# Performance work log

Hardware: AMD Instinct MI355X
Metric: run time of the kernel (lower is better)

Reference implementation:

```python
import jax, jax.numpy as jnp
import numpy as np

D = 512          # input_dim == hidden size of MinLSTM layers
OUT = 1          # output_dim of fc_out
B, T = 8, 4096
LN_EPS = 1e-5


def _linear_params(key, d_in, d_out):
    kw, kb = jax.random.split(key)
    lim = 1.0 / np.sqrt(d_in)
    W = jax.random.uniform(kw, (d_out, d_in), minval=-lim, maxval=lim, dtype=jnp.float32)
    b = jax.random.uniform(kb, (d_out,), minval=-lim, maxval=lim, dtype=jnp.float32)
    return W, b


def setup_inputs() -> dict:
    key = jax.random.key(0)
    ks = jax.random.split(key, 8)
    x = jax.random.normal(ks[0], (B, T, D), dtype=jnp.float32)
    Wf0, bf0 = _linear_params(ks[1], D, D)
    Wi0, bi0 = _linear_params(ks[2], D, D)
    Wh0, bh0 = _linear_params(ks[3], D, D)
    Wf1, bf1 = _linear_params(ks[4], D, D)
    Wi1, bi1 = _linear_params(ks[5], D, D)
    Wh1, bh1 = _linear_params(ks[6], D, D)
    W_out, b_out = _linear_params(ks[7], D, OUT)
    ln_g = jnp.ones((D,), dtype=jnp.float32)
    ln_b = jnp.zeros((D,), dtype=jnp.float32)
    return {
        'x': x,
        'Wf0': Wf0, 'bf0': bf0, 'Wi0': Wi0, 'bi0': bi0, 'Wh0': Wh0, 'bh0': bh0,
        'Wf1': Wf1, 'bf1': bf1, 'Wi1': Wi1, 'bi1': bi1, 'Wh1': Wh1, 'bh1': bh1,
        'ln_g': ln_g, 'ln_b': ln_b, 'W_out': W_out, 'b_out': b_out,
    }


def _minlstm(x, Wf, bf, Wi, bi, Wh, bh):
    # minLSTM (parallel form, h0 = 0):
    #   f = sigma(W_f x), i = sigma(W_i x), h~ = W_h x
    #   f' = f/(f+i), i' = i/(f+i)
    #   h_t = f'_t * h_{t-1} + i'_t * h~_t   (linear recurrence -> associative scan)
    f = jax.nn.sigmoid(jnp.einsum('btd,ed->bte', x, Wf) + bf)
    i = jax.nn.sigmoid(jnp.einsum('btd,ed->bte', x, Wi) + bi)
    h_tilde = jnp.einsum('btd,ed->bte', x, Wh) + bh
    denom = f + i
    a = f / denom                      # decay coefficient f'
    u = (i / denom) * h_tilde          # input contribution i' * h~

    def combine(c1, c2):
        a1, u1 = c1
        a2, u2 = c2
        return a1 * a2, a2 * u1 + u2

    _, h = jax.lax.associative_scan(combine, (a, u), axis=1)
    return h  # [B, T, D]


def reference(x, Wf0, bf0, Wi0, bi0, Wh0, bh0,
              Wf1, bf1, Wi1, bi1, Wh1, bh1,
              ln_g, ln_b, W_out, b_out):
    h = _minlstm(x, Wf0, bf0, Wi0, bi0, Wh0, bh0)
    h = _minlstm(h, Wf1, bf1, Wi1, bi1, Wh1, bh1)
    h = jnp.where(jnp.isnan(h), x, h)      # NaN fallback to input
    h = x + h                               # residual
    # LayerNorm over last dim
    mu = jnp.mean(h, axis=-1, keepdims=True)
    var = jnp.mean(jnp.square(h - mu), axis=-1, keepdims=True)
    hn = (h - mu) * jax.lax.rsqrt(var + LN_EPS) * ln_g + ln_b
    # output projection [B, T, OUT]
    return jnp.einsum('btd,od->bto', hn, W_out) + b_out
```

## Files before the change

### kernel.cpp

```cpp
#include <hip/hip_runtime.h>
#include <hip/hip_bf16.h>
#include <stdint.h>


#define MROWS 32768
#define DDIM  512
#define TLEN  4096
#define BSZ   8
#define NCHUNK 64
#define CLEN   64

typedef __attribute__((ext_vector_type(8))) __bf16 bf16x8;
typedef __attribute__((ext_vector_type(4))) float f32x4;
typedef __attribute__((ext_vector_type(4))) unsigned short ushort4_t;

static __device__ __forceinline__ unsigned short f2bf(float f) {
    unsigned int u = __float_as_uint(f);
    u = (u + 0x7FFFu + ((u >> 16) & 1u)) >> 16;
    return (unsigned short)u;
}
static __device__ __forceinline__ float bf2f(unsigned short s) {
    return __uint_as_float(((unsigned int)s) << 16);
}
static __device__ __forceinline__ void gload_lds16(const void* gptr, void* ldsp) {
    __builtin_amdgcn_global_load_lds(
        (const __attribute__((address_space(1))) uint32_t*)gptr,
        (__attribute__((address_space(3))) uint32_t*)ldsp,
        16, 0, 0);
}

#define WAITV(n) asm volatile("s_waitcnt vmcnt(" #n ")" ::: "memory")

__global__ __launch_bounds__(256) void cast_all(
    const float4* __restrict__ x,
    const float4* __restrict__ w0, const float4* __restrict__ w1,
    const float4* __restrict__ w2, const float4* __restrict__ w3,
    const float4* __restrict__ w4, const float4* __restrict__ w5,
    ushort4_t* __restrict__ xb, ushort4_t* __restrict__ wb)
{
    int i = blockIdx.x * 256 + threadIdx.x;
    float4 v;
    ushort4_t* dst;
    if (i < 4194304) {
        v = x[i];
        dst = xb + i;
    } else {
        int j = i - 4194304;
        int wsel = j >> 16;
        int rem = j & 65535;
        const float4* src = (wsel == 0) ? w0 : (wsel == 1) ? w1 : (wsel == 2) ? w2
                          : (wsel == 3) ? w3 : (wsel == 4) ? w4 : w5;
        v = src[rem];
        dst = wb + j;
    }
    ushort4_t o;
    o.x = f2bf(v.x); o.y = f2bf(v.y); o.z = f2bf(v.z); o.w = f2bf(v.w);
    *dst = o;
}

__global__ __launch_bounds__(512, 4) void gates_gemm(
    const unsigned short* __restrict__ X,
    const unsigned short* __restrict__ Wf,
    const unsigned short* __restrict__ Wi,
    const unsigned short* __restrict__ Wh,
    const float* __restrict__ bf_, const float* __restrict__ bi_,
    const float* __restrict__ bh_,
    unsigned int* __restrict__ au_out,
    float* __restrict__ Asum, float* __restrict__ Usum)
{
    __shared__ __align__(16) unsigned short lds[2 * 10240];

    const int tid  = threadIdx.x;
    const int lane = tid & 63;
    const int wave = tid >> 6;
    const int wm = wave >> 1;
    const int wn = wave & 1;
    const int lr  = lane & 15;
    const int kgl = lane >> 4;

    const int w = blockIdx.x;
    const int xcd = w & 7;
    const int s = w >> 3;
    const int by = xcd * 32 + (s >> 3);
    const int bx = s & 7;
    const int mblk = by * 128;
    const int nblk = bx * 64;

    const int r4 = lane >> 2;
    const int c4 = lane & 3;
    const unsigned short *g0, *g1, *g2;
    int o0, o1, o2;
    {
        const int sb = (wave < 4) ? wave * 3 : 12 + (wave - 4) * 2;
        const int sl2 = (wave < 4) ? sb + 2 : sb + 1;
        const int sls[3] = {sb, sb + 1, sl2};
        const unsigned short* gp[3];
        int of[3];
#pragma unroll
        for (int i = 0; i < 3; ++i) {
            int sl = sls[i];
            const unsigned short* src;
            int lrow, grow;
            if (sl < 8)       { src = X;  lrow = sl * 16 + r4;        grow = mblk + lrow; }
            else if (sl < 12) { src = Wf; lrow = (sl - 8) * 16 + r4;  grow = nblk + lrow; }
            else if (sl < 16) { src = Wi; lrow = (sl - 12) * 16 + r4; grow = nblk + lrow; }
            else              { src = Wh; lrow = (sl - 16) * 16 + r4; grow = nblk + lrow; }
            int cg = ((c4 ^ (lrow >> 1)) & 3) << 3;
            gp[i] = src + (size_t)grow * 512 + cg;
            of[i] = sl * 512 + r4 * 32 + c4 * 8;
        }
        g0 = gp[0]; g1 = gp[1]; g2 = gp[2];
        o0 = of[0]; o1 = of[1]; o2 = of[2];
    }

    int aoff[2], boff[2];
#pragma unroll
    for (int mi = 0; mi < 2; ++mi) {
        int row = wm * 32 + mi * 16 + lr;
        aoff[mi] = row * 32 + (((kgl ^ (row >> 1)) & 3) << 3);
    }
#pragma unroll
    for (int ni = 0; ni < 2; ++ni) {
        int row = wn * 32 + ni * 16 + lr;
        boff[ni] = 4096 + row * 32 + (((kgl ^ (row >> 1)) & 3) << 3);
    }

    f32x4 accF[2][2], accI[2][2], accH[2][2];
    const f32x4 zero = {0.f, 0.f, 0.f, 0.f};
#pragma unroll
    for (int mi = 0; mi < 2; ++mi)
#pragma unroll
        for (int ni = 0; ni < 2; ++ni) {
            accF[mi][ni] = zero; accI[mi][ni] = zero; accH[mi][ni] = zero;
        }

#define STAGE(bb) do { \
    gload_lds16(g0, lds + (bb) + o0); \
    gload_lds16(g1, lds + (bb) + o1); \
    if (wave < 4) gload_lds16(g2, lds + (bb) + o2); \
    g0 += 32; g1 += 32; g2 += 32; } while (0)

    STAGE(0);

#pragma unroll
    for (int t = 0; t < 16; ++t) {
        if (t < 15) {
            STAGE(((t + 1) & 1) * 10240);
            if (wave < 4) { WAITV(3); } else { WAITV(2); }
        } else {
            WAITV(0);
        }
        __builtin_amdgcn_s_barrier();
        __builtin_amdgcn_sched_barrier(0);

        const unsigned short* cb = lds + (t & 1) * 10240;
        bf16x8 af[2];
#pragma unroll
        for (int mi = 0; mi < 2; ++mi)
            af[mi] = *reinterpret_cast<const bf16x8*>(cb + aoff[mi]);
        bf16x8 bF[2], bI[2], bH[2];
#pragma unroll
        for (int ni = 0; ni < 2; ++ni) {
            bF[ni] = *reinterpret_cast<const bf16x8*>(cb + boff[ni]);
            bI[ni] = *reinterpret_cast<const bf16x8*>(cb + 2048 + boff[ni]);
            bH[ni] = *reinterpret_cast<const bf16x8*>(cb + 4096 + boff[ni]);
        }
        __builtin_amdgcn_s_setprio(1);
#pragma unroll
        for (int mi = 0; mi < 2; ++mi)
#pragma unroll
            for (int ni = 0; ni < 2; ++ni) {
                accF[mi][ni] = __builtin_amdgcn_mfma_f32_16x16x32_bf16(af[mi], bF[ni], accF[mi][ni], 0, 0, 0);
                accI[mi][ni] = __builtin_amdgcn_mfma_f32_16x16x32_bf16(af[mi], bI[ni], accI[mi][ni], 0, 0, 0);
                accH[mi][ni] = __builtin_amdgcn_mfma_f32_16x16x32_bf16(af[mi], bH[ni], accH[mi][ni], 0, 0, 0);
            }
        __builtin_amdgcn_s_setprio(0);
        __builtin_amdgcn_sched_barrier(0);
        __builtin_amdgcn_s_barrier();
        __builtin_amdgcn_sched_barrier(0);
    }
#undef STAGE

    float pa[2], pu[2];
#pragma unroll
    for (int ni = 0; ni < 2; ++ni) {
        const int n = nblk + wn * 32 + ni * 16 + lr;
        const float bfv = bf_[n], biv = bi_[n], bhv = bh_[n];
        float ca = 1.f, cu = 0.f;
#pragma unroll
        for (int mi = 0; mi < 2; ++mi) {
            float sa = 1.f, su = 0.f;
#pragma unroll
            for (int r = 0; r < 4; ++r) {
                const int m = mblk + wm * 32 + mi * 16 + kgl * 4 + r;
                float zf = accF[mi][ni][r] + bfv;
                float zi = accI[mi][ni][r] + biv;
                float zh = accH[mi][ni][r] + bhv;
                float ef = __expf(-zf);
                float ei = __expf(-zi);
                float inv = __frcp_rn(2.0f + ef + ei);
                float av = (1.0f + ei) * inv;
                float uv = (1.0f + ef) * inv * zh;
                au_out[(size_t)m * 512 + n] =
                    ((unsigned int)f2bf(uv) << 16) | (unsigned int)f2bf(av);
                sa *= av; su = av * su + uv;
            }
            float oa = __shfl_xor(sa, 16), ou = __shfl_xor(su, 16);
            bool up = (lane & 16) != 0;
            float ta = sa * oa;
            float tu = up ? (sa * ou + su) : (oa * su + ou);
            sa = ta; su = tu;
            oa = __shfl_xor(sa, 32); ou = __shfl_xor(su, 32);
            up = (lane & 32) != 0;
            ta = sa * oa;
            tu = up ? (sa * ou + su) : (oa * su + ou);
            sa = ta; su = tu;
            cu = sa * cu + su; ca = ca * sa;
        }
        pa[ni] = ca; pu[ni] = cu;
    }
    float* sm = (float*)lds;
    if (kgl == 0) {
#pragma unroll
        for (int ni = 0; ni < 2; ++ni) {
            int nl = wn * 32 + ni * 16 + lr;
            sm[wm * 64 + nl] = pa[ni];
            sm[256 + wm * 64 + nl] = pu[ni];
        }
    }
    __syncthreads();
    if (tid < 128) {
        int cl = tid >> 6, nl = tid & 63;
        float a1 = sm[(2 * cl) * 64 + nl],     u1 = sm[256 + (2 * cl) * 64 + nl];
        float a2 = sm[(2 * cl + 1) * 64 + nl], u2 = sm[256 + (2 * cl + 1) * 64 + nl];
        size_t ci = (size_t)(by * 2 + cl) * 512 + nblk + nl;
        Asum[ci] = a1 * a2;
        Usum[ci] = a2 * u1 + u2;
    }
}

__global__ void scan_pass2(const float4* __restrict__ Asum, const float4* __restrict__ Usum,
                           float4* __restrict__ Hinit) {
    int t = blockIdx.x * 256 + threadIdx.x;
    int d4 = t & 127;
    int b = t >> 7;
    float4 h = {0.f, 0.f, 0.f, 0.f};
    for (int c = 0; c < NCHUNK; ++c) {
        size_t idx = (size_t)(b * NCHUNK + c) * 128 + d4;
        Hinit[idx] = h;
        float4 A = Asum[idx]; float4 U = Usum[idx];
        h.x = A.x * h.x + U.x; h.y = A.y * h.y + U.y;
        h.z = A.z * h.z + U.z; h.w = A.w * h.w + U.w;
    }
}

__global__ void scan_pass3(const uint4* __restrict__ au,
                           const float4* __restrict__ Hinit,
                           ushort4_t* __restrict__ hout) {
    int gid = blockIdx.x * 256 + threadIdx.x;
    int d4 = gid & 127;
    int c  = (gid >> 7) & 63;
    int b  = gid >> 13;
    size_t base = (size_t)(b * TLEN + c * CLEN) * 128 + d4;
    size_t s4 = (size_t)(b * NCHUNK + c) * 128 + d4;
    float4 h0 = Hinit[s4];
    float h[4] = {h0.x, h0.y, h0.z, h0.w};
#pragma unroll 4
    for (int l = 0; l < CLEN; ++l) {
        size_t idx = base + (size_t)l * 128;
        uint4 v = au[idx];
        unsigned int vv[4] = {v.x, v.y, v.z, v.w};
        ushort4_t o;
#pragma unroll
        for (int j = 0; j < 4; ++j) {
            float av = __uint_as_float(vv[j] << 16);
            float uv = __uint_as_float(vv[j] & 0xFFFF0000u);
            h[j] = av * h[j] + uv;
            o[j] = f2bf(h[j]);
        }
        hout[idx] = o;
    }
}

__global__ __launch_bounds__(128) void scan3_final(
    const uint4* __restrict__ au, const float4* __restrict__ Hinit,
    const float4* __restrict__ x4,
    const float* __restrict__ g, const float* __restrict__ bvec,
    const float* __restrict__ Wout, const float* __restrict__ bout,
    float* __restrict__ out)
{
    const int blk = blockIdx.x;
    const int b = blk >> 6, c = blk & 63;
    const int d4 = threadIdx.x;
    const int lane = threadIdx.x & 63;
    const int wv = threadIdx.x >> 6;

    float4 h0 = Hinit[(size_t)blk * 128 + d4];
    float h[4] = {h0.x, h0.y, h0.z, h0.w};
    float4 g4 = reinterpret_cast<const float4*>(g)[d4];
    float4 b4 = reinterpret_cast<const float4*>(bvec)[d4];
    float4 w4 = reinterpret_cast<const float4*>(Wout)[d4];
    const float ga[4] = {g4.x, g4.y, g4.z, g4.w};
    const float ba[4] = {b4.x, b4.y, b4.z, b4.w};
    const float wa[4] = {w4.x, w4.y, w4.z, w4.w};
    const float bo = bout[0];

    __shared__ float redS[2], redQ[2], redP[2];
    size_t base = ((size_t)b * TLEN + c * CLEN) * 128 + d4;

    for (int l = 0; l < CLEN; ++l) {
        size_t idx = base + (size_t)l * 128;
        uint4 v = au[idx];
        float4 xr = x4[idx];
        const unsigned int vv[4] = {v.x, v.y, v.z, v.w};
        const float xa[4] = {xr.x, xr.y, xr.z, xr.w};
        float r[4];
        float sfl = 0.f, q = 0.f;
#pragma unroll
        for (int j = 0; j < 4; ++j) {
            float av = __uint_as_float(vv[j] << 16);
            float uv = __uint_as_float(vv[j] & 0xFFFF0000u);
            h[j] = av * h[j] + uv;
            float hv = h[j];
            if (hv != hv) hv = xa[j];
            float rr = xa[j] + hv;
            r[j] = rr;
            sfl += rr; q += rr * rr;
        }
#pragma unroll
        for (int m = 32; m >= 1; m >>= 1) {
            sfl += __shfl_xor(sfl, m);
            q += __shfl_xor(q, m);
        }
        if (lane == 0) { redS[wv] = sfl; redQ[wv] = q; }
        __syncthreads();
        float st = redS[0] + redS[1];
        float qt = redQ[0] + redQ[1];
        float mu = st * (1.0f / 512.0f);
        float var = qt * (1.0f / 512.0f) - mu * mu;
        float rstd = rsqrtf(var + 1e-5f);
        float p = 0.f;
#pragma unroll
        for (int j = 0; j < 4; ++j)
            p += ((r[j] - mu) * rstd * ga[j] + ba[j]) * wa[j];
#pragma unroll
        for (int m = 32; m >= 1; m >>= 1) p += __shfl_xor(p, m);
        if (lane == 0) redP[wv] = p;
        __syncthreads();
        if (threadIdx.x == 0)
            out[(size_t)b * TLEN + c * CLEN + l] = redP[0] + redP[1] + bo;
    }
}

extern "C" void kernel_launch(void* const* d_in, const int* in_sizes, int n_in,
                              void* d_out, int out_size, void* d_ws, size_t ws_size,
                              hipStream_t stream) {
    const float* x    = (const float*)d_in[0];
    const float* Wf0  = (const float*)d_in[1];  const float* bf0 = (const float*)d_in[2];
    const float* Wi0  = (const float*)d_in[3];  const float* bi0 = (const float*)d_in[4];
    const float* Wh0  = (const float*)d_in[5];  const float* bh0 = (const float*)d_in[6];
    const float* Wf1  = (const float*)d_in[7];  const float* bf1 = (const float*)d_in[8];
    const float* Wi1  = (const float*)d_in[9];  const float* bi1 = (const float*)d_in[10];
    const float* Wh1  = (const float*)d_in[11]; const float* bh1 = (const float*)d_in[12];
    const float* ln_g = (const float*)d_in[13]; const float* ln_b = (const float*)d_in[14];
    const float* W_out = (const float*)d_in[15]; const float* b_out = (const float*)d_in[16];

    char* ws = (char*)d_ws;
    unsigned short* Xb = (unsigned short*)ws;  ws += (size_t)MROWS * DDIM * 2;
    unsigned short* Wball = (unsigned short*)ws;
    unsigned short* Wb[6];
    for (int i = 0; i < 6; ++i) { Wb[i] = (unsigned short*)ws; ws += (size_t)DDIM * DDIM * 2; }
    unsigned int* aubuf = (unsigned int*)ws; ws += (size_t)MROWS * DDIM * 4;
    float* Asum = (float*)ws;  ws += (size_t)BSZ * NCHUNK * DDIM * 4;
    float* Usum = (float*)ws;  ws += (size_t)BSZ * NCHUNK * DDIM * 4;
    float* Hinit = (float*)ws; ws += (size_t)BSZ * NCHUNK * DDIM * 4;
    unsigned short* h0b = (unsigned short*)ws; ws += (size_t)MROWS * DDIM * 2;

    cast_all<<<17920, 256, 0, stream>>>(
        (const float4*)x, (const float4*)Wf0, (const float4*)Wi0, (const float4*)Wh0,
        (const float4*)Wf1, (const float4*)Wi1, (const float4*)Wh1,
        (ushort4_t*)Xb, (ushort4_t*)Wball);

    gates_gemm<<<2048, 512, 0, stream>>>(Xb, Wb[0], Wb[1], Wb[2], bf0, bi0, bh0,
                                         aubuf, Asum, Usum);
    scan_pass2<<<4, 256, 0, stream>>>((const float4*)Asum, (const float4*)Usum, (float4*)Hinit);
    scan_pass3<<<256, 256, 0, stream>>>((const uint4*)aubuf, (const float4*)Hinit, (ushort4_t*)h0b);

    gates_gemm<<<2048, 512, 0, stream>>>(h0b, Wb[3], Wb[4], Wb[5], bf1, bi1, bh1,
                                         aubuf, Asum, Usum);
    scan_pass2<<<4, 256, 0, stream>>>((const float4*)Asum, (const float4*)Usum, (float4*)Hinit);
    scan3_final<<<512, 128, 0, stream>>>((const uint4*)aubuf, (const float4*)Hinit,
                                         (const float4*)x, ln_g, ln_b, W_out, b_out,
                                         (float*)d_out);
}
```

Baseline: 246.5 us.

## Switch gates GEMM to 32x32x16 MFMA with 4 waves per block

Rewrites the gates GEMM to use 256-thread blocks (4 waves), with each wave computing a 64x32 tile via 32x32x16 bf16 MFMA instead of 16x16x32, and restructures LDS staging so each thread issues five uniform 16-byte loads. Each wave now owns a full 64-row chunk, so the chunk scan summary is written straight from registers without the shared-memory combine and extra block barrier. The aim is fewer LDS fragment reads per FLOP and less epilogue sync. The cost is more accumulator registers per wave and fewer waves per block for latency hiding.

```diff
diff --git a/kernel.cpp b/kernel.cpp
--- a/kernel.cpp
+++ b/kernel.cpp
@@ -11,7 +11,7 @@
 #define CLEN   64
 
 typedef __attribute__((ext_vector_type(8))) __bf16 bf16x8;
-typedef __attribute__((ext_vector_type(4))) float f32x4;
+typedef __attribute__((ext_vector_type(16))) float f32x16;
 typedef __attribute__((ext_vector_type(4))) unsigned short ushort4_t;
 
 static __device__ __forceinline__ unsigned short f2bf(float f) {
@@ -58,7 +58,7 @@
     *dst = o;
 }
 
-__global__ __launch_bounds__(512, 4) void gates_gemm(
+__global__ __launch_bounds__(256, 3) void gates_gemm(
     const unsigned short* __restrict__ X,
     const unsigned short* __restrict__ Wf,
     const unsigned short* __restrict__ Wi,
@@ -75,8 +75,8 @@
     const int wave = tid >> 6;
     const int wm = wave >> 1;
     const int wn = wave & 1;
-    const int lr  = lane & 15;
-    const int kgl = lane >> 4;
+    const int ln31 = lane & 31;
+    const int kh = lane >> 5;
 
     const int w = blockIdx.x;
     const int xcd = w & 7;
@@ -86,59 +86,45 @@
     const int mblk = by * 128;
     const int nblk = bx * 64;
 
-    const int r4 = lane >> 2;
-    const int c4 = lane & 3;
-    const unsigned short *g0, *g1, *g2;
-    int o0, o1, o2;
+    const int srow = tid >> 2;
+    const int c4   = tid & 3;
+    const int cg   = ((c4 ^ ((srow >> 1) & 3)) << 3);
+    const int tid8 = tid * 8;
+    const unsigned short* g0 = X  + (size_t)(mblk + srow) * 512 + cg;
+    const unsigned short* g1 = X  + (size_t)(mblk + 64 + srow) * 512 + cg;
+    const unsigned short* g2 = Wf + (size_t)(nblk + srow) * 512 + cg;
+    const unsigned short* g3 = Wi + (size_t)(nblk + srow) * 512 + cg;
+    const unsigned short* g4 = Wh + (size_t)(nblk + srow) * 512 + cg;
+
+    int aoff[2][2], boff[2];
+#pragma unroll
+    for (int mi = 0; mi < 2; ++mi) {
+        int row = wm * 64 + mi * 32 + ln31;
+#pragma unroll
+        for (int ks = 0; ks < 2; ++ks)
+            aoff[mi][ks] = row * 32 + (((2 * ks + kh) ^ ((row >> 1) & 3)) << 3);
+    }
     {
-        const int sb = (wave < 4) ? wave * 3 : 12 + (wave - 4) * 2;
-        const int sl2 = (wave < 4) ? sb + 2 : sb + 1;
-        const int sls[3] = {sb, sb + 1, sl2};
-        const unsigned short* gp[3];
-        int of[3];
-#pragma unroll
-        for (int i = 0; i < 3; ++i) {
-            int sl = sls[i];
-            const unsigned short* src;
-            int lrow, grow;
-            if (sl < 8)       { src = X;  lrow = sl * 16 + r4;        grow = mblk + lrow; }
-            else if (sl < 12) { src = Wf; lrow = (sl - 8) * 16 + r4;  grow = nblk + lrow; }
-            else if (sl < 16) { src = Wi; lrow = (sl - 12) * 16 + r4; grow = nblk + lrow; }
-            else              { src = Wh; lrow = (sl - 16) * 16 + r4; grow = nblk + lrow; }
-            int cg = ((c4 ^ (lrow >> 1)) & 3) << 3;
-            gp[i] = src + (size_t)grow * 512 + cg;
-            of[i] = sl * 512 + r4 * 32 + c4 * 8;
-        }
-        g0 = gp[0]; g1 = gp[1]; g2 = gp[2];
-        o0 = of[0]; o1 = of[1]; o2 = of[2];
-    }
-
-    int aoff[2], boff[2];
+        int brow = wn * 32 + ln31;
+#pragma unroll
+        for (int ks = 0; ks < 2; ++ks)
+            boff[ks] = brow * 32 + (((2 * ks + kh) ^ ((brow >> 1) & 3)) << 3);
+    }
+
+    f32x16 accF[2], accI[2], accH[2];
 #pragma unroll
     for (int mi = 0; mi < 2; ++mi) {
-        int row = wm * 32 + mi * 16 + lr;
-        aoff[mi] = row * 32 + (((kgl ^ (row >> 1)) & 3) << 3);
-    }
-#pragma unroll
-    for (int ni = 0; ni < 2; ++ni) {
-        int row = wn * 32 + ni * 16 + lr;
-        boff[ni] = 4096 + row * 32 + (((kgl ^ (row >> 1)) & 3) << 3);
-    }
-
-    f32x4 accF[2][2], accI[2][2], accH[2][2];
-    const f32x4 zero = {0.f, 0.f, 0.f, 0.f};
-#pragma unroll
-    for (int mi = 0; mi < 2; ++mi)
-#pragma unroll
-        for (int ni = 0; ni < 2; ++ni) {
-            accF[mi][ni] = zero; accI[mi][ni] = zero; accH[mi][ni] = zero;
-        }
+#pragma unroll
+        for (int e = 0; e < 16; ++e) { accF[mi][e] = 0.f; accI[mi][e] = 0.f; accH[mi][e] = 0.f; }
+    }
 
 #define STAGE(bb) do { \
-    gload_lds16(g0, lds + (bb) + o0); \
-    gload_lds16(g1, lds + (bb) + o1); \
-    if (wave < 4) gload_lds16(g2, lds + (bb) + o2); \
-    g0 += 32; g1 += 32; g2 += 32; } while (0)
+    gload_lds16(g0, lds + (bb) + tid8);            \
+    gload_lds16(g1, lds + (bb) + 2048 + tid8);     \
+    gload_lds16(g2, lds + (bb) + 4096 + tid8);     \
+    gload_lds16(g3, lds + (bb) + 6144 + tid8);     \
+    gload_lds16(g4, lds + (bb) + 8192 + tid8);     \
+    g0 += 32; g1 += 32; g2 += 32; g3 += 32; g4 += 32; } while (0)
 
     STAGE(0);
 
@@ -146,7 +132,7 @@
     for (int t = 0; t < 16; ++t) {
         if (t < 15) {
             STAGE(((t + 1) & 1) * 10240);
-            if (wave < 4) { WAITV(3); } else { WAITV(2); }
+            WAITV(5);
         } else {
             WAITV(0);
         }
@@ -154,48 +140,45 @@
         __builtin_amdgcn_sched_barrier(0);
 
         const unsigned short* cb = lds + (t & 1) * 10240;
-        bf16x8 af[2];
-#pragma unroll
-        for (int mi = 0; mi < 2; ++mi)
-            af[mi] = *reinterpret_cast<const bf16x8*>(cb + aoff[mi]);
-        bf16x8 bF[2], bI[2], bH[2];
-#pragma unroll
-        for (int ni = 0; ni < 2; ++ni) {
-            bF[ni] = *reinterpret_cast<const bf16x8*>(cb + boff[ni]);
-            bI[ni] = *reinterpret_cast<const bf16x8*>(cb + 2048 + boff[ni]);
-            bH[ni] = *reinterpret_cast<const bf16x8*>(cb + 4096 + boff[ni]);
-        }
-        __builtin_amdgcn_s_setprio(1);
-#pragma unroll
-        for (int mi = 0; mi < 2; ++mi)
-#pragma unroll
-            for (int ni = 0; ni < 2; ++ni) {
-                accF[mi][ni] = __builtin_amdgcn_mfma_f32_16x16x32_bf16(af[mi], bF[ni], accF[mi][ni], 0, 0, 0);
-                accI[mi][ni] = __builtin_amdgcn_mfma_f32_16x16x32_bf16(af[mi], bI[ni], accI[mi][ni], 0, 0, 0);
-                accH[mi][ni] = __builtin_amdgcn_mfma_f32_16x16x32_bf16(af[mi], bH[ni], accH[mi][ni], 0, 0, 0);
+#pragma unroll
+        for (int ks = 0; ks < 2; ++ks) {
+            bf16x8 af[2];
+            af[0] = *reinterpret_cast<const bf16x8*>(cb + aoff[0][ks]);
+            af[1] = *reinterpret_cast<const bf16x8*>(cb + aoff[1][ks]);
+            bf16x8 bF = *reinterpret_cast<const bf16x8*>(cb + 4096 + boff[ks]);
+            bf16x8 bI = *reinterpret_cast<const bf16x8*>(cb + 6144 + boff[ks]);
+            bf16x8 bH = *reinterpret_cast<const bf16x8*>(cb + 8192 + boff[ks]);
+            __builtin_amdgcn_s_setprio(1);
+#pragma unroll
+            for (int mi = 0; mi < 2; ++mi) {
+                accF[mi] = __builtin_amdgcn_mfma_f32_32x32x16_bf16(af[mi], bF, accF[mi], 0, 0, 0);
+                accI[mi] = __builtin_amdgcn_mfma_f32_32x32x16_bf16(af[mi], bI, accI[mi], 0, 0, 0);
+                accH[mi] = __builtin_amdgcn_mfma_f32_32x32x16_bf16(af[mi], bH, accH[mi], 0, 0, 0);
             }
-        __builtin_amdgcn_s_setprio(0);
+            __builtin_amdgcn_s_setprio(0);
+        }
         __builtin_amdgcn_sched_barrier(0);
         __builtin_amdgcn_s_barrier();
         __builtin_amdgcn_sched_barrier(0);
     }
 #undef STAGE
 
-    float pa[2], pu[2];
-#pragma unroll
-    for (int ni = 0; ni < 2; ++ni) {
-        const int n = nblk + wn * 32 + ni * 16 + lr;
-        const float bfv = bf_[n], biv = bi_[n], bhv = bh_[n];
-        float ca = 1.f, cu = 0.f;
-#pragma unroll
-        for (int mi = 0; mi < 2; ++mi) {
+    const int n = nblk + wn * 32 + ln31;
+    const float bfv = bf_[n], biv = bi_[n], bhv = bh_[n];
+    const bool up = (lane & 32) != 0;
+    float ca = 1.f, cu = 0.f;
+#pragma unroll
+    for (int mi = 0; mi < 2; ++mi) {
+#pragma unroll
+        for (int j = 0; j < 4; ++j) {
             float sa = 1.f, su = 0.f;
 #pragma unroll
             for (int r = 0; r < 4; ++r) {
-                const int m = mblk + wm * 32 + mi * 16 + kgl * 4 + r;
-                float zf = accF[mi][ni][r] + bfv;
-                float zi = accI[mi][ni][r] + biv;
-                float zh = accH[mi][ni][r] + bhv;
+                const int reg = 4 * j + r;
+                const int m = mblk + wm * 64 + mi * 32 + 8 * j + 4 * kh + r;
+                float zf = accF[mi][reg] + bfv;
+                float zi = accI[mi][reg] + biv;
+                float zh = accH[mi][reg] + bhv;
                 float ef = __expf(-zf);
                 float ei = __expf(-zi);
                 float inv = __frcp_rn(2.0f + ef + ei);
@@ -203,39 +186,18 @@
                 float uv = (1.0f + ef) * inv * zh;
                 au_out[(size_t)m * 512 + n] =
                     ((unsigned int)f2bf(uv) << 16) | (unsigned int)f2bf(av);
-                sa *= av; su = av * su + uv;
+                su = av * su + uv; sa *= av;
             }
-            float oa = __shfl_xor(sa, 16), ou = __shfl_xor(su, 16);
-            bool up = (lane & 16) != 0;
+            float oa = __shfl_xor(sa, 32), ou = __shfl_xor(su, 32);
             float ta = sa * oa;
             float tu = up ? (sa * ou + su) : (oa * su + ou);
-            sa = ta; su = tu;
-            oa = __shfl_xor(sa, 32); ou = __shfl_xor(su, 32);
-            up = (lane & 32) != 0;
-            ta = sa * oa;
-            tu = up ? (sa * ou + su) : (oa * su + ou);
-            sa = ta; su = tu;
-            cu = sa * cu + su; ca = ca * sa;
-        }
-        pa[ni] = ca; pu[ni] = cu;
-    }
-    float* sm = (float*)lds;
-    if (kgl == 0) {
-#pragma unroll
-        for (int ni = 0; ni < 2; ++ni) {
-            int nl = wn * 32 + ni * 16 + lr;
-            sm[wm * 64 + nl] = pa[ni];
-            sm[256 + wm * 64 + nl] = pu[ni];
-        }
-    }
-    __syncthreads();
-    if (tid < 128) {
-        int cl = tid >> 6, nl = tid & 63;
-        float a1 = sm[(2 * cl) * 64 + nl],     u1 = sm[256 + (2 * cl) * 64 + nl];
-        float a2 = sm[(2 * cl + 1) * 64 + nl], u2 = sm[256 + (2 * cl + 1) * 64 + nl];
-        size_t ci = (size_t)(by * 2 + cl) * 512 + nblk + nl;
-        Asum[ci] = a1 * a2;
-        Usum[ci] = a2 * u1 + u2;
+            cu = ta * cu + tu; ca = ca * ta;
+        }
+    }
+    if (lane < 32) {
+        size_t ci = (size_t)(by * 2 + wm) * 512 + n;
+        Asum[ci] = ca;
+        Usum[ci] = cu;
     }
 }
 
@@ -381,12 +343,12 @@
         (const float4*)Wf1, (const float4*)Wi1, (const float4*)Wh1,
         (ushort4_t*)Xb, (ushort4_t*)Wball);
 
-    gates_gemm<<<2048, 512, 0, stream>>>(Xb, Wb[0], Wb[1], Wb[2], bf0, bi0, bh0,
+    gates_gemm<<<2048, 256, 0, stream>>>(Xb, Wb[0], Wb[1], Wb[2], bf0, bi0, bh0,
                                          aubuf, Asum, Usum);
     scan_pass2<<<4, 256, 0, stream>>>((const float4*)Asum, (const float4*)Usum, (float4*)Hinit);
     scan_pass3<<<256, 256, 0, stream>>>((const uint4*)aubuf, (const float4*)Hinit, (ushort4_t*)h0b);
 
-    gates_gemm<<<2048, 512, 0, stream>>>(h0b, Wb[3], Wb[4], Wb[5], bf1, bi1, bh1,
+    gates_gemm<<<2048, 256, 0, stream>>>(h0b, Wb[3], Wb[4], Wb[5], bf1, bi1, bh1,
                                          aubuf, Asum, Usum);
     scan_pass2<<<4, 256, 0, stream>>>((const float4*)Asum, (const float4*)Usum, (float4*)Hinit);
     scan3_final<<<512, 128, 0, stream>>>((const uint4*)aubuf, (const float4*)Hinit,
```

Measured after the change: 246.2 us. About the same (-0.1%).
